# Kernel tuning notes

Hardware: AMD Instinct MI355X
Metric: run time of the kernel (lower is better)

## Reference

```python
import jax, jax.numpy as jnp
import numpy as np

IN_CH = 32
OUT_CH = 32
M1, M2 = 32, 32
BS, H, W = 8, 256, 256


def setup_inputs() -> dict:
    key = jax.random.key(0)
    kx, kk = jax.random.split(key)
    x = jax.random.normal(kx, (BS, IN_CH, H, W), dtype=jnp.float32)
    # reset_parameters: randn * (1/(in_ch*out_ch)) + 1
    scale = 1.0 / (IN_CH * OUT_CH)
    kernel = jax.random.normal(kk, (2, 1, OUT_CH, M1, M2, 2), dtype=jnp.float32) * scale + 1.0
    r = jnp.float32(1.0)
    return {"x": x, "kernel": kernel, "r": r}


def reference(x, kernel, r):
    # view_as_complex: last dim of 2 -> complex, shape [2, 1, C, M1, M2]
    kc = (kernel[..., 0] + 1j * kernel[..., 1]).astype(jnp.complex64)
    # elementwise complex power kernel**r
    kc = jnp.power(kc, r)

    # forward 2D real FFT over spatial dims (ortho norm)
    x_ft = jnp.fft.rfftn(x, axes=(-2, -1), norm="ortho")  # [bs, C, H, W//2+1]
    Hf, Wr = x_ft.shape[-2], x_ft.shape[-1]
    n1 = min(Hf // 2, M1)
    n2 = min(Wr, M2)

    def mix(block, k):
        # fft over channel dim (-3), multiply by complex kernel, ifft back
        b = jnp.fft.fft(block, axis=-3, norm="ortho")
        b = b * k[..., :n1, :n2]
        return jnp.fft.ifft(b, axis=-3, norm="ortho")

    pos = mix(x_ft[..., :n1, :n2], kc[0])          # low positive freqs
    neg = mix(x_ft[..., Hf - n1:, :n2], kc[1])     # low negative freqs

    out_ft = jnp.zeros((x.shape[0], OUT_CH, Hf, Wr), dtype=jnp.complex64)
    out_ft = out_ft.at[..., :n1, :n2].set(pos)
    out_ft = out_ft.at[..., Hf - n1:, :n2].set(neg)

    # inverse real FFT back to spatial domain
    return jnp.fft.irfftn(out_ft, s=(x.shape[-2], x.shape[-1]), axes=(-2, -1), norm="ortho")
```

## Files before the change

### kernel.cpp

```cpp
#include <hip/hip_runtime.h>
#include <math.h>


#define TWO_PI 6.28318530717958647692f

__global__ __launch_bounds__(256) void kP(const float* __restrict__ kin,
                                          const float* __restrict__ rp,
                                          float2* __restrict__ kp) {
  const int i = blockIdx.x * 256 + threadIdx.x;
  const float r = rp[0];
  const float kr = kin[2 * i], ki = kin[2 * i + 1];
  const float m2 = fmaf(kr, kr, ki * ki);
  float2 o = make_float2(0.f, 0.f);
  if (m2 > 0.f) {
    const float lm = 0.5f * logf(m2);
    const float ang = atan2f(ki, kr);
    const float mag = expf(r * lm);
    float s, c;
    sincosf(r * ang, &s, &c);
    o = make_float2(mag * c, mag * s);
  }
  kp[i] = o;
}

__global__ __launch_bounds__(256) void kA(const float* __restrict__ x,
                                          float2* __restrict__ z1) {
  __shared__ float xs[8192];
  const int tid = threadIdx.x;
  const long row0 = (long)blockIdx.x * 32;
  const float* xg = x + row0 * 256;
  {
    const int xl = tid & 31, rq = tid >> 5;
    const float* xgr = xg + rq * 4 * 256 + xl;
#pragma unroll
    for (int cb = 0; cb < 8; ++cb) {
      const int xc = xl + 32 * cb;
      const float4 v = make_float4(xgr[32 * cb], xgr[32 * cb + 256],
                                   xgr[32 * cb + 512], xgr[32 * cb + 768]);
      *(float4*)(xs + xc * 32 + 4 * ((rq + xc) & 7)) = v;
    }
  }
  __syncthreads();
  const float RT = 0.70710678118654752440f;
#pragma unroll
  for (int k = 0; k < 4; ++k) {
    const int i = tid + (k << 8);
    const int x1 = i >> 5, r = i & 31;
    float* base = xs + x1 * 32 + ((r + 4 * x1) & 31);
    const float a0 = base[0],        a1 = base[1024],     a2 = base[2048];
    const float a3 = base[3 * 1024], a4 = base[4 * 1024], a5 = base[5 * 1024];
    const float a6 = base[6 * 1024], a7 = base[7 * 1024];
    const float t0 = a0 + a4, t1 = a0 - a4, t2 = a2 + a6, t3 = a2 - a6;
    const float u0 = a1 + a5, u1 = a1 - a5, u2 = a3 + a7, u3 = a3 - a7;
    const float E0 = t0 + t2, O0 = u0 + u2;
    const float d1 = RT * (u1 - u3), d2 = RT * (u1 + u3);
    base[0]        = E0 + O0;
    base[1024]     = E0 - O0;
    base[2 * 1024] = t1 + d1;
    base[3 * 1024] = -(t3 + d2);
    base[4 * 1024] = t0 - t2;
    base[5 * 1024] = -(u0 - u2);
    base[6 * 1024] = t1 - d1;
    base[7 * 1024] = t3 - d2;
  }
  __syncthreads();
  const int w = tid & 31;
  const int r0 = (tid >> 5) << 2;
  const int p = w & 7;
  int pr, pi;
  float si;
  if (p == 0)      { pr = 0;           pi = 0;      si = 0.f; }
  else if (p == 4) { pr = 1;           pi = 1;      si = 0.f; }
  else if (p < 4)  { pr = 2 * p;       pi = pr + 1; si = 1.f; }
  else             { pr = 2 * (8 - p); pi = pr + 1; si = -1.f; }
  const char* ur = (const char*)xs + pr * 4096;
  const char* ui = (const char*)xs + pi * 4096;
  const char* urp[8];
  const char* uip[8];
#pragma unroll
  for (int j = 0; j < 8; ++j) {
    const int off = 4 * ((r0 + 4 * j) & 31) + 128 * j;
    urp[j] = ur + off;
    uip[j] = ui + off;
  }
  float s1, c1;
  sincosf(-TWO_PI * (float)w / 256.0f, &s1, &c1);
  float pc = 1.f, ps = 0.f;
  float Cr0 = 0, Cr1 = 0, Cr2 = 0, Cr3 = 0;
  float Ci0 = 0, Ci1 = 0, Ci2 = 0, Ci3 = 0;
#pragma unroll
  for (int bq = 0; bq < 4; ++bq) {
#pragma unroll
    for (int j = 0; j < 8; ++j) {
      const float4 Fr = *(const float4*)(urp[j] + bq * 1024);
      const float4 Fi = *(const float4*)(uip[j] + bq * 1024);
      const float qs = si * ps, qc = si * pc;
      Cr0 = fmaf(Fr.x, pc, fmaf(-Fi.x, qs, Cr0));
      Ci0 = fmaf(Fr.x, ps, fmaf( Fi.x, qc, Ci0));
      Cr1 = fmaf(Fr.y, pc, fmaf(-Fi.y, qs, Cr1));
      Ci1 = fmaf(Fr.y, ps, fmaf( Fi.y, qc, Ci1));
      Cr2 = fmaf(Fr.z, pc, fmaf(-Fi.z, qs, Cr2));
      Ci2 = fmaf(Fr.z, ps, fmaf( Fi.z, qc, Ci2));
      Cr3 = fmaf(Fr.w, pc, fmaf(-Fi.w, qs, Cr3));
      Ci3 = fmaf(Fr.w, ps, fmaf( Fi.w, qc, Ci3));
      const float tn = fmaf(pc, c1, -ps * s1);
      ps = fmaf(pc, s1, ps * c1);
      pc = tn;
    }
  }
  float2* o = z1 + (row0 + r0) * 32 + w;
  o[0]  = make_float2(Cr0, Ci0);
  o[32] = make_float2(Cr1, Ci1);
  o[64] = make_float2(Cr2, Ci2);
  o[96] = make_float2(Cr3, Ci3);
}

__global__ __launch_bounds__(256) void kB(const float2* __restrict__ z1,
                                          float2* __restrict__ z2) {
  __shared__ float2 zs[8192];
  const int tid = threadIdx.x;
  const int bc = blockIdx.x >> 1, th = blockIdx.x & 1;
  {
    const float4* s4 = (const float4*)(z1 + (long)bc * 8192);
    float4* d4 = (float4*)zs;
    for (int i = tid; i < 4096; i += 256) d4[i] = s4[i];
  }
  __syncthreads();
  const float RT = 0.70710678118654752440f;
#pragma unroll
  for (int e = 0; e < 4; ++e) {
    float2* base = zs + tid + (e << 8);
    float2 a[8];
#pragma unroll
    for (int j = 0; j < 8; ++j) a[j] = base[j * 1024];
    float2 t0 = make_float2(a[0].x + a[4].x, a[0].y + a[4].y);
    float2 t1 = make_float2(a[0].x - a[4].x, a[0].y - a[4].y);
    float2 t2 = make_float2(a[2].x + a[6].x, a[2].y + a[6].y);
    float2 t3 = make_float2(a[2].x - a[6].x, a[2].y - a[6].y);
    const float2 E0 = make_float2(t0.x + t2.x, t0.y + t2.y);
    const float2 E2 = make_float2(t0.x - t2.x, t0.y - t2.y);
    const float2 E1 = make_float2(t1.x + t3.y, t1.y - t3.x);
    const float2 E3 = make_float2(t1.x - t3.y, t1.y + t3.x);
    t0 = make_float2(a[1].x + a[5].x, a[1].y + a[5].y);
    t1 = make_float2(a[1].x - a[5].x, a[1].y - a[5].y);
    t2 = make_float2(a[3].x + a[7].x, a[3].y + a[7].y);
    t3 = make_float2(a[3].x - a[7].x, a[3].y - a[7].y);
    const float2 O0 = make_float2(t0.x + t2.x, t0.y + t2.y);
    const float2 O2 = make_float2(t0.x - t2.x, t0.y - t2.y);
    const float2 O1 = make_float2(t1.x + t3.y, t1.y - t3.x);
    const float2 O3 = make_float2(t1.x - t3.y, t1.y + t3.x);
    const float2 B0 = O0;
    const float2 B1 = make_float2(RT * (O1.x + O1.y), RT * (O1.y - O1.x));
    const float2 B2 = make_float2(O2.y, -O2.x);
    const float2 B3 = make_float2(RT * (O3.y - O3.x), -RT * (O3.x + O3.y));
    base[0]        = make_float2(E0.x + B0.x, E0.y + B0.y);
    base[1 * 1024] = make_float2(E1.x + B1.x, E1.y + B1.y);
    base[2 * 1024] = make_float2(E2.x + B2.x, E2.y + B2.y);
    base[3 * 1024] = make_float2(E3.x + B3.x, E3.y + B3.y);
    base[4 * 1024] = make_float2(E0.x - B0.x, E0.y - B0.y);
    base[5 * 1024] = make_float2(E1.x - B1.x, E1.y - B1.y);
    base[6 * 1024] = make_float2(E2.x - B2.x, E2.y - B2.y);
    base[7 * 1024] = make_float2(E3.x - B3.x, E3.y - B3.y);
  }
  __syncthreads();
  const int w = tid & 31;
  const int lt = tid >> 5;
  const int t0i = th * 32 + lt;
  const int hbase = th ? (192 + t0i) : t0i;
  float stc[4], sts[4], pcq[4], psq[4], ar[4], ai[4];
#pragma unroll
  for (int q = 0; q < 4; ++q) {
    sincosf(-TWO_PI * (float)(hbase + 8 * q) / 256.0f, &sts[q], &stc[q]);
    pcq[q] = 1.f; psq[q] = 0.f; ar[q] = 0.f; ai[q] = 0.f;
  }
  const float2* sp = zs + lt * 1024 + w;
  for (int y1 = 0; y1 < 32; ++y1) {
    const float2 v = sp[y1 * 32];
#pragma unroll
    for (int q = 0; q < 4; ++q) {
      ar[q] = fmaf(v.x, pcq[q], fmaf(-v.y, psq[q], ar[q]));
      ai[q] = fmaf(v.x, psq[q], fmaf( v.y, pcq[q], ai[q]));
      const float tn = fmaf(pcq[q], stc[q], -psq[q] * sts[q]);
      psq[q] = fmaf(pcq[q], sts[q], psq[q] * stc[q]);
      pcq[q] = tn;
    }
  }
  float2* dst = z2 + (long)bc * 2048 + t0i * 32 + w;
#pragma unroll
  for (int q = 0; q < 4; ++q) dst[q * 256] = make_float2(ar[q], ai[q]);
}

__global__ __launch_bounds__(256) void kC(const float2* __restrict__ z2,
                                          const float2* __restrict__ kp,
                                          float2* __restrict__ g) {
  __shared__ float2 z2s[8 * 33];
  __shared__ float2 fk[8 * 33];
  __shared__ float2 tw[32];
  const int tid = threadIdx.x;
  if (tid < 32) {
    float s, c;
    sincosf(-TWO_PI * (float)tid / 32.0f, &s, &c);
    tw[tid] = make_float2(c, s);
  }
  const int m0 = blockIdx.x * 8;
  const int b = m0 >> 11;
  const int twi = m0 & 2047;
  const int t = twi >> 5;
  const int w0 = twi & 31;
  const int s_ = t >> 5, tm = t & 31;
  {
    const int ci = tid >> 3, wj = tid & 7;
    z2s[wj * 33 + ci] = z2[((long)(b * 32 + ci)) * 2048 + t * 32 + w0 + wj];
  }
  __syncthreads();
  const int m = tid & 7;
  {
    const int cf = tid >> 3;
    float fr = 0, fi = 0;
    int i0 = 0;
#pragma unroll 8
    for (int ci = 0; ci < 32; ++ci) {
      const float2 z = z2s[m * 33 + ci];
      const float2 t0 = tw[i0]; i0 = (i0 + cf) & 31;
      fr = fmaf(z.x, t0.x, fmaf(-z.y, t0.y, fr));
      fi = fmaf(z.x, t0.y, fmaf( z.y, t0.x, fi));
    }
    const float2 k0 = kp[((s_ * 32 + cf) * 32 + tm) * 32 + w0 + m];
    fk[m * 33 + cf] = make_float2(fr * k0.x - fi * k0.y, fr * k0.y + fi * k0.x);
  }
  __syncthreads();
  {
    const int co = tid >> 3;
    float gr = 0, gi = 0;
    int i0 = 0;
#pragma unroll 8
    for (int cf = 0; cf < 32; ++cf) {
      const float2 f = fk[m * 33 + cf];
      const float2 t0 = tw[i0]; i0 = (i0 + co) & 31;
      gr = fmaf(f.x, t0.x, fmaf( f.y, t0.y, gr));
      gi = fmaf(f.y, t0.x, fmaf(-f.x, t0.y, gi));
    }
    const float SC = 1.0f / 8192.0f;
    g[((long)(b * 32 + co)) * 2048 + t * 32 + w0 + m] = make_float2(gr * SC, gi * SC);
  }
}

__global__ __launch_bounds__(512) void kDE2(const float2* __restrict__ g,
                                            float* __restrict__ out) {
  __shared__ float2 gs[2048];
  __shared__ float2 tst[32 * 34];
  const int tid = threadIdx.x;
  const int bc = blockIdx.x >> 1, yh = blockIdx.x & 1;
  {
    const float4* s4 = (const float4*)(g + (long)bc * 2048);
    float4* d4 = (float4*)gs;
    for (int i = tid; i < 1024; i += 512) d4[i] = s4[i];
  }
  __syncthreads();
  const int w = tid & 31;
  float Ur[2][8], Ui[2][8];
#pragma unroll
  for (int e = 0; e < 2; ++e) {
    const int y1 = (tid + (e << 9)) >> 5;
#pragma unroll
    for (int p = 0; p < 8; ++p) { Ur[e][p] = 0.f; Ui[e][p] = 0.f; }
    float s1, c1;
    sincosf(TWO_PI * (float)y1 / 256.0f, &s1, &c1);
    float pc = 1.f, ps = 0.f;
#pragma unroll
    for (int t = 0; t < 64; ++t) {
      if (t == 32) {
        float s2, c2;
        sincosf(TWO_PI * (float)((224 * y1) & 255) / 256.0f, &s2, &c2);
        pc = c2; ps = s2;
      }
      const float2 v = gs[t * 32 + w];
      const int k = t & 7;
      Ur[e][k] = fmaf(v.x, pc, fmaf(-v.y, ps, Ur[e][k]));
      Ui[e][k] = fmaf(v.x, ps, fmaf( v.y, pc, Ui[e][k]));
      const float tn = fmaf(pc, c1, -ps * s1);
      ps = fmaf(pc, s1, ps * c1);
      pc = tn;
    }
  }
  const int xq = tid & 31;
  const int rh = tid >> 5;
  float sb, cb;
  sincosf(TWO_PI * (float)xq / 256.0f, &sb, &cb);
  const float RT = 0.70710678118654752440f;
  const float stc1 = RT * (cb - sb), sts1 = RT * (cb + sb);
  const float stcx[4] = {cb, stc1, -sb, -sts1};
  const float stsx[4] = {sb, sts1, cb, stc1};
  const long rb0 = (long)bc * 256;
#pragma unroll
  for (int yql = 0; yql < 4; ++yql) {
    const int yq = yh * 4 + yql;
    {
      float sqv, cqv;
      sincosf(TWO_PI * (float)yq / 8.0f, &sqv, &cqv);
#pragma unroll
      for (int e = 0; e < 2; ++e) {
        const int y1 = (tid + (e << 9)) >> 5;
        float tr = 0.f, ti = 0.f, qc = 1.f, qs = 0.f;
#pragma unroll
        for (int p = 0; p < 8; ++p) {
          tr = fmaf(Ur[e][p], qc, fmaf(-Ui[e][p], qs, tr));
          ti = fmaf(Ur[e][p], qs, fmaf( Ui[e][p], qc, ti));
          const float tn = fmaf(qc, cqv, -qs * sqv);
          qs = fmaf(qc, sqv, qs * cqv);
          qc = tn;
        }
        const float sc = w ? (2.0f / 256.0f) : (1.0f / 256.0f);
        tst[w * 34 + y1] = make_float2(tr * sc, ti * sc);
      }
    }
    __syncthreads();
    {
      float C[4][2], S[4][2];
#pragma unroll
      for (int m = 0; m < 4; ++m) {
        C[m][0] = 0.f; C[m][1] = 0.f; S[m][0] = 0.f; S[m][1] = 0.f;
      }
      float pcx[4] = {1.f, 1.f, 1.f, 1.f}, psx[4] = {0.f, 0.f, 0.f, 0.f};
      const float* tbse = (const float*)tst + rh * 4;
#pragma unroll 2
      for (int w2 = 0; w2 < 32; ++w2) {
        const float4 q0 = *(const float4*)(tbse + w2 * 68);
#pragma unroll
        for (int m = 0; m < 4; ++m) {
          C[m][0] = fmaf(q0.x, pcx[m], C[m][0]);
          S[m][0] = fmaf(q0.y, psx[m], S[m][0]);
          C[m][1] = fmaf(q0.z, pcx[m], C[m][1]);
          S[m][1] = fmaf(q0.w, psx[m], S[m][1]);
          const float tn = fmaf(pcx[m], stcx[m], -psx[m] * stsx[m]);
          psx[m] = fmaf(pcx[m], stsx[m], psx[m] * stcx[m]);
          pcx[m] = tn;
        }
      }
      const long rbase = rb0 + yq * 32;
#pragma unroll
      for (int m = 0; m < 4; ++m) {
        const int xx = xq + 32 * m;
#pragma unroll
        for (int j = 0; j < 2; ++j) {
          const long row = rbase + rh * 2 + j;
          out[row * 256 + xx] = C[m][j] - S[m][j];
          out[row * 256 + ((256 - xx) & 255)] = C[m][j] + S[m][j];
        }
      }
      if (tid < 32) {
        float ae = 0.f, ao = 0.f;
#pragma unroll
        for (int k = 0; k < 16; ++k) {
          ae += tst[(2 * k) * 34 + tid].x;
          ao += tst[(2 * k + 1) * 34 + tid].x;
        }
        out[(rbase + tid) * 256 + 128] = ae - ao;
      }
    }
    __syncthreads();
  }
}

extern "C" void kernel_launch(void* const* d_in, const int* in_sizes, int n_in,
                              void* d_out, int out_size, void* d_ws, size_t ws_size,
                              hipStream_t stream) {
  const float* x = (const float*)d_in[0];
  const float* kin = (const float*)d_in[1];
  const float* rp = (const float*)d_in[2];
  float* out = (float*)d_out;
  char* ws = (char*)d_ws;

  float2* z1 = (float2*)(ws);
  float2* z2 = (float2*)(ws + (16ull << 20));
  float2* kp = (float2*)(ws + (24ull << 20));
  float2* g  = (float2*)(ws);

  kP<<<256, 256, 0, stream>>>(kin, rp, kp);
  kA<<<2048, 256, 0, stream>>>(x, z1);
  kB<<<512, 256, 0, stream>>>(z1, z2);
  kC<<<2048, 256, 0, stream>>>(z2, kp, g);
  kDE2<<<512, 512, 0, stream>>>(g, out);
}
```

Measured before the change: 197.8 us.

## Compute final inverse real DFT along width with fp16 MFMA against precomputed twiddle matrix

The final width-direction inverse real DFT in kDE2 was a scalar FMA loop with a twiddle recurrence and split cos/sin outputs. It now runs as a 32x256 matrix product on MFMA 16x16x32 f16. A new kernel kX precomputes the fp16 cos/-sin twiddle matrix with the scaling folded in, and intermediate spectra are stored to LDS as fp16. This removes ALU work but lowers intermediate precision to fp16, which risks accuracy, and adds a small extra launch.

```diff
diff --git a/kernel.cpp b/kernel.cpp
--- a/kernel.cpp
+++ b/kernel.cpp
@@ -3,6 +3,9 @@
 
 
 #define TWO_PI 6.28318530717958647692f
+
+typedef _Float16 half8 __attribute__((ext_vector_type(8)));
+typedef float float4v __attribute__((ext_vector_type(4)));
 
 __global__ __launch_bounds__(256) void kP(const float* __restrict__ kin,
                                           const float* __restrict__ rp,
@@ -21,6 +24,25 @@
     o = make_float2(mag * c, mag * s);
   }
   kp[i] = o;
+}
+
+__global__ __launch_bounds__(256) void kX(_Float16* __restrict__ Bf) {
+  const int f0 = (blockIdx.x * 256 + threadIdx.x) * 2;
+#pragma unroll
+  for (int u = 0; u < 2; ++u) {
+    const int f = f0 + u;
+    const int i = f & 7;
+    const int lane = (f >> 3) & 63;
+    const int kk = (f >> 9) & 1;
+    const int n = f >> 10;
+    const int k = kk * 32 + ((lane >> 4) << 3) + i;
+    const int w = k >> 1, cs = k & 1;
+    const int xc = n * 16 + (lane & 15);
+    const float sc = (w ? 2.0f : 1.0f) / 256.0f;
+    float s, c;
+    sincosf(TWO_PI * (float)((w * xc) & 255) / 256.0f, &s, &c);
+    Bf[f] = (_Float16)(cs ? (-s * sc) : (c * sc));
+  }
 }
 
 __global__ __launch_bounds__(256) void kA(const float* __restrict__ x,
@@ -246,11 +268,21 @@
 }
 
 __global__ __launch_bounds__(512) void kDE2(const float2* __restrict__ g,
+                                            const _Float16* __restrict__ Bf,
                                             float* __restrict__ out) {
   __shared__ float2 gs[2048];
-  __shared__ float2 tst[32 * 34];
+  __shared__ _Float16 tst2[32 * 68];
   const int tid = threadIdx.x;
   const int bc = blockIdx.x >> 1, yh = blockIdx.x & 1;
+  const int lane = tid & 63, l15 = lane & 15, lg = lane >> 4;
+  uint4 bfr[2][2];
+#pragma unroll
+  for (int nn = 0; nn < 2; ++nn)
+#pragma unroll
+    for (int kk = 0; kk < 2; ++kk) {
+      const int n = 2 * (tid >> 6) + nn;
+      bfr[nn][kk] = *(const uint4*)(Bf + (((n * 2 + kk) * 64) + lane) * 8);
+    }
   {
     const float4* s4 = (const float4*)(g + (long)bc * 2048);
     float4* d4 = (float4*)gs;
@@ -283,14 +315,6 @@
       pc = tn;
     }
   }
-  const int xq = tid & 31;
-  const int rh = tid >> 5;
-  float sb, cb;
-  sincosf(TWO_PI * (float)xq / 256.0f, &sb, &cb);
-  const float RT = 0.70710678118654752440f;
-  const float stc1 = RT * (cb - sb), sts1 = RT * (cb + sb);
-  const float stcx[4] = {cb, stc1, -sb, -sts1};
-  const float stsx[4] = {sb, sts1, cb, stc1};
   const long rb0 = (long)bc * 256;
 #pragma unroll
   for (int yql = 0; yql < 4; ++yql) {
@@ -310,53 +334,44 @@
           qs = fmaf(qc, sqv, qs * cqv);
           qc = tn;
         }
-        const float sc = w ? (2.0f / 256.0f) : (1.0f / 256.0f);
-        tst[w * 34 + y1] = make_float2(tr * sc, ti * sc);
+        union { unsigned int u; _Float16 h[2]; } hu;
+        hu.h[0] = (_Float16)tr;
+        hu.h[1] = (_Float16)ti;
+        *(unsigned int*)&tst2[y1 * 68 + 2 * w] = hu.u;
       }
     }
     __syncthreads();
     {
-      float C[4][2], S[4][2];
-#pragma unroll
-      for (int m = 0; m < 4; ++m) {
-        C[m][0] = 0.f; C[m][1] = 0.f; S[m][0] = 0.f; S[m][1] = 0.f;
-      }
-      float pcx[4] = {1.f, 1.f, 1.f, 1.f}, psx[4] = {0.f, 0.f, 0.f, 0.f};
-      const float* tbse = (const float*)tst + rh * 4;
-#pragma unroll 2
-      for (int w2 = 0; w2 < 32; ++w2) {
-        const float4 q0 = *(const float4*)(tbse + w2 * 68);
-#pragma unroll
-        for (int m = 0; m < 4; ++m) {
-          C[m][0] = fmaf(q0.x, pcx[m], C[m][0]);
-          S[m][0] = fmaf(q0.y, psx[m], S[m][0]);
-          C[m][1] = fmaf(q0.z, pcx[m], C[m][1]);
-          S[m][1] = fmaf(q0.w, psx[m], S[m][1]);
-          const float tn = fmaf(pcx[m], stcx[m], -psx[m] * stsx[m]);
-          psx[m] = fmaf(pcx[m], stsx[m], psx[m] * stcx[m]);
-          pcx[m] = tn;
+      half8 afr[2][2];
+#pragma unroll
+      for (int rt = 0; rt < 2; ++rt)
+#pragma unroll
+        for (int kk = 0; kk < 2; ++kk) {
+          const _Float16* ap = tst2 + (rt * 16 + l15) * 68 + kk * 32 + lg * 8;
+          const uint2 lo = *(const uint2*)ap;
+          const uint2 hi = *(const uint2*)(ap + 4);
+          uint4 u4;
+          u4.x = lo.x; u4.y = lo.y; u4.z = hi.x; u4.w = hi.y;
+          afr[rt][kk] = __builtin_bit_cast(half8, u4);
         }
-      }
       const long rbase = rb0 + yq * 32;
 #pragma unroll
-      for (int m = 0; m < 4; ++m) {
-        const int xx = xq + 32 * m;
-#pragma unroll
-        for (int j = 0; j < 2; ++j) {
-          const long row = rbase + rh * 2 + j;
-          out[row * 256 + xx] = C[m][j] - S[m][j];
-          out[row * 256 + ((256 - xx) & 255)] = C[m][j] + S[m][j];
+      for (int rt = 0; rt < 2; ++rt)
+#pragma unroll
+        for (int nn = 0; nn < 2; ++nn) {
+          float4v acc = {0.f, 0.f, 0.f, 0.f};
+          acc = __builtin_amdgcn_mfma_f32_16x16x32_f16(
+              afr[rt][0], __builtin_bit_cast(half8, bfr[nn][0]), acc, 0, 0, 0);
+          acc = __builtin_amdgcn_mfma_f32_16x16x32_f16(
+              afr[rt][1], __builtin_bit_cast(half8, bfr[nn][1]), acc, 0, 0, 0);
+          const int n = 2 * (tid >> 6) + nn;
+          const int col = n * 16 + l15;
+          const long r0w = rbase + rt * 16 + lg * 4;
+          out[(r0w + 0) * 256 + col] = acc[0];
+          out[(r0w + 1) * 256 + col] = acc[1];
+          out[(r0w + 2) * 256 + col] = acc[2];
+          out[(r0w + 3) * 256 + col] = acc[3];
         }
-      }
-      if (tid < 32) {
-        float ae = 0.f, ao = 0.f;
-#pragma unroll
-        for (int k = 0; k < 16; ++k) {
-          ae += tst[(2 * k) * 34 + tid].x;
-          ao += tst[(2 * k + 1) * 34 + tid].x;
-        }
-        out[(rbase + tid) * 256 + 128] = ae - ao;
-      }
     }
     __syncthreads();
   }
@@ -374,11 +389,13 @@
   float2* z1 = (float2*)(ws);
   float2* z2 = (float2*)(ws + (16ull << 20));
   float2* kp = (float2*)(ws + (24ull << 20));
+  _Float16* Bf = (_Float16*)(ws + (25ull << 20));
   float2* g  = (float2*)(ws);
 
   kP<<<256, 256, 0, stream>>>(kin, rp, kp);
+  kX<<<32, 256, 0, stream>>>(Bf);
   kA<<<2048, 256, 0, stream>>>(x, z1);
   kB<<<512, 256, 0, stream>>>(z1, z2);
   kC<<<2048, 256, 0, stream>>>(z2, kp, g);
-  kDE2<<<512, 512, 0, stream>>>(g, out);
-}
+  kDE2<<<512, 512, 0, stream>>>(g, Bf, out);
+}
```

Measured after the change: 185.2 us. -6.3%, faster.
